# Kernel optimization log

Hardware: AMD Instinct MI355X
Metric: run time of the kernel (lower is better)

Reference implementation:

```python
import jax, jax.numpy as jnp
import numpy as np
import math

D_MODEL = 1024
NUM_HEADS = 16
D_KV = 64
INNER = NUM_HEADS * D_KV
NUM_BUCKETS = 32
MAX_DISTANCE = 128


def _relative_position_bucket(relative_position, num_buckets=NUM_BUCKETS, max_distance=MAX_DISTANCE):
    # bidirectional T5 bucketing
    n = -relative_position
    num_buckets = num_buckets // 2
    ret = (n < 0).astype(jnp.int32) * num_buckets
    n = jnp.abs(n)
    max_exact = num_buckets // 2
    is_small = n < max_exact
    n_safe = jnp.maximum(n, 1).astype(jnp.float32)  # avoid log(0); masked by is_small
    val_if_large = max_exact + (
        jnp.log(n_safe / max_exact) / math.log(max_distance / max_exact) * (num_buckets - max_exact)
    ).astype(jnp.int32)
    val_if_large = jnp.minimum(val_if_large, num_buckets - 1)
    return jnp.where(is_small, n, val_if_large) + ret


def _position_bias(rel_emb, q_len, k_len):
    ctx = jnp.arange(q_len)[:, None]
    mem = jnp.arange(k_len)[None, :]
    buckets = _relative_position_bucket(mem - ctx)          # [q, k]
    values = rel_emb[buckets]                               # [q, k, H]
    return jnp.transpose(values, (2, 0, 1))[None]           # [1, H, q, k]


def setup_inputs() -> dict:
    key = jax.random.key(0)
    ks = jax.random.split(key, 6)
    B, S = 2, 2048
    scale = 1.0 / math.sqrt(D_MODEL)
    return {
        "hidden_states": jax.random.normal(ks[0], (B, S, D_MODEL), dtype=jnp.float32),
        "mask": jnp.zeros((B, 1, 1, S), dtype=jnp.float32),
        "Wq": jax.random.normal(ks[1], (D_MODEL, INNER), dtype=jnp.float32) * scale,
        "Wk": jax.random.normal(ks[2], (D_MODEL, INNER), dtype=jnp.float32) * scale,
        "Wv": jax.random.normal(ks[3], (D_MODEL, INNER), dtype=jnp.float32) * scale,
        "Wo": jax.random.normal(ks[4], (INNER, D_MODEL), dtype=jnp.float32) * scale,
        "rel_emb": jax.random.normal(ks[5], (NUM_BUCKETS, NUM_HEADS), dtype=jnp.float32),
    }


def reference(hidden_states, mask, Wq, Wk, Wv, Wo, rel_emb):
    B, S, _ = hidden_states.shape
    def split_heads(x):
        return jnp.transpose(x.reshape(B, -1, NUM_HEADS, D_KV), (0, 2, 1, 3))  # [B,H,S,d]
    q = split_heads(hidden_states @ Wq)
    k = split_heads(hidden_states @ Wk)
    v = split_heads(hidden_states @ Wv)
    scores = jnp.einsum("bhqd,bhkd->bhqk", q, k)            # unscaled, T5-style
    position_bias = _position_bias(rel_emb, S, S)           # [1,H,S,S]
    scores = scores + position_bias + mask
    attn = jax.nn.softmax(scores, axis=-1)
    context = jnp.einsum("bhqk,bhkd->bhqd", attn, v)
    context = jnp.transpose(context, (0, 2, 1, 3)).reshape(B, S, INNER)
    output = context @ Wo
    return output, position_bias
```

## Files before the change

kernel.cpp:

```cpp
#include <hip/hip_runtime.h>
#include <cstdint>

#define AS1 __attribute__((address_space(1)))
#define AS3 __attribute__((address_space(3)))

typedef _Float16 half8 __attribute__((ext_vector_type(8)));
typedef _Float16 half4_t __attribute__((ext_vector_type(4)));
typedef float v4f __attribute__((ext_vector_type(4)));

__device__ __forceinline__ void async_ld16(const void* g, void* l) {
  __builtin_amdgcn_global_load_lds((const AS1 uint32_t*)g, (AS3 uint32_t*)l, 16, 0, 0);
}

__device__ __forceinline__ int t5_bucket(int delta) {
  int n = -delta;
  int ret = 0;
  if (n < 0) { ret = 16; n = -n; }
  if (n < 8) return n + ret;
  if (n >= 91) return 15 + ret;
  if ((n & (n - 1)) == 0) {
    int l = 31 - __clz(n);
    int v = 2 + 2 * l;
    return (v > 15 ? 15 : v) + ret;
  }
  int v = 8 + (int)(logf((float)n * 0.125f) * (8.0f / logf(16.0f)));
  return (v > 15 ? 15 : v) + ret;
}

__global__ void k_cvt(const float* __restrict__ src, _Float16* __restrict__ dst) {
  int t = blockIdx.x * 256 + threadIdx.x;
  float4 f = ((const float4*)src)[t];
  half4_t h = {(_Float16)f.x, (_Float16)f.y, (_Float16)f.z, (_Float16)f.w};
  ((half4_t*)dst)[t] = h;
}

__global__ void k_wt(const float* __restrict__ src, _Float16* __restrict__ dst) {
  __shared__ float tile[32][33];
  int tx = threadIdx.x, ty = threadIdx.y;
  int bx = blockIdx.x * 32, by = blockIdx.y * 32;
#pragma unroll
  for (int i = 0; i < 32; i += 8)
    tile[ty + i][tx] = src[(size_t)(by + ty + i) * 1024 + bx + tx];
  __syncthreads();
#pragma unroll
  for (int i = 0; i < 32; i += 8)
    dst[(size_t)(bx + ty + i) * 1024 + by + tx] = (_Float16)tile[tx][ty + i];
}

__global__ void k_vt(const _Float16* __restrict__ qkv, _Float16* __restrict__ vT) {
  __shared__ float tile[64 * 73];
  const int t = threadIdx.x;
  const int s0 = blockIdx.x * 64, h = blockIdx.y, b = blockIdx.z;
  const int r = t >> 2, c = (t & 3) * 16;
  const _Float16* src = qkv + (size_t)(b * 2048 + s0 + r) * 3072 + 2048 + h * 64 + c;
  half8 a0 = *(const half8*)src;
  half8 a1 = *(const half8*)(src + 8);
#pragma unroll
  for (int e = 0; e < 8; ++e) tile[r * 73 + c + e] = (float)a0[e];
#pragma unroll
  for (int e = 0; e < 8; ++e) tile[r * 73 + c + 8 + e] = (float)a1[e];
  __syncthreads();
  half8 w0, w1;
#pragma unroll
  for (int e = 0; e < 8; ++e) w0[e] = (_Float16)tile[(c + e) * 73 + r];
#pragma unroll
  for (int e = 0; e < 8; ++e) w1[e] = (_Float16)tile[(c + 8 + e) * 73 + r];
  _Float16* dst = vT + ((size_t)((b * 16 + h) * 64 + r)) * 2048 + s0 + c;
  *(half8*)dst = w0;
  *(half8*)(dst + 8) = w1;
}

__global__ void k_bias(const float* __restrict__ rel, float* __restrict__ outb) {
  __shared__ float tbl[512];
  int tid = threadIdx.x;
  tbl[tid] = rel[tid];
  tbl[tid + 256] = rel[tid + 256];
  __syncthreads();
  unsigned t = blockIdx.x * 256 + tid;
  int k4 = t & 511;
  int q = (t >> 9) & 2047;
  int h = t >> 20;
  int kb = k4 * 4;
  float4 v;
  if (kb - q >= 91) {
    float c = tbl[31 * 16 + h];
    v = make_float4(c, c, c, c);
  } else if (q - kb - 3 >= 91) {
    float c = tbl[15 * 16 + h];
    v = make_float4(c, c, c, c);
  } else {
    v.x = tbl[t5_bucket(kb + 0 - q) * 16 + h];
    v.y = tbl[t5_bucket(kb + 1 - q) * 16 + h];
    v.z = tbl[t5_bucket(kb + 2 - q) * 16 + h];
    v.w = tbl[t5_bucket(kb + 3 - q) * 16 + h];
  }
  ((float4*)outb)[((size_t)h * 2048 + q) * 512 + k4] = v;
}

template <bool F16OUT>
__global__ __launch_bounds__(256, 2) void k_gemm(const _Float16* __restrict__ A,
                                                 const _Float16* __restrict__ BT,
                                                 void* __restrict__ Cv, int K, int ldc) {
  __shared__ __align__(16) _Float16 As[128 * 32];
  __shared__ __align__(16) _Float16 Bs[128 * 32];
  const int tid = threadIdx.x;
  const int wave = tid >> 6, lane = tid & 63;
  const int l15 = lane & 15, quad = lane >> 4;
  const int m0 = blockIdx.y * 128, n0 = blockIdx.x * 128;
  const int wm = (wave >> 1) * 64, wn = (wave & 1) * 64;
  const int r0 = tid >> 2, c0 = (tid & 3) * 8;
  v4f acc[4][4] = {};
  for (int k0 = 0; k0 < K; k0 += 32) {
    __syncthreads();
    async_ld16(A + (size_t)(m0 + r0) * K + k0 + c0, (char*)As + (size_t)(wave * 64) * 16);
    async_ld16(A + (size_t)(m0 + 64 + r0) * K + k0 + c0,
               (char*)As + (size_t)(256 + wave * 64) * 16);
    async_ld16(BT + (size_t)(n0 + r0) * K + k0 + c0, (char*)Bs + (size_t)(wave * 64) * 16);
    async_ld16(BT + (size_t)(n0 + 64 + r0) * K + k0 + c0,
               (char*)Bs + (size_t)(256 + wave * 64) * 16);
    __syncthreads();
    half8 af[4], bf[4];
#pragma unroll
    for (int mt = 0; mt < 4; ++mt)
      af[mt] = *(const half8*)(As + (wm + mt * 16 + l15) * 32 + quad * 8);
#pragma unroll
    for (int nt = 0; nt < 4; ++nt)
      bf[nt] = *(const half8*)(Bs + (wn + nt * 16 + l15) * 32 + quad * 8);
#pragma unroll
    for (int mt = 0; mt < 4; ++mt)
#pragma unroll
      for (int nt = 0; nt < 4; ++nt)
        acc[mt][nt] = __builtin_amdgcn_mfma_f32_16x16x32_f16(af[mt], bf[nt], acc[mt][nt], 0, 0, 0);
  }
#pragma unroll
  for (int mt = 0; mt < 4; ++mt)
#pragma unroll
    for (int nt = 0; nt < 4; ++nt)
#pragma unroll
      for (int r = 0; r < 4; ++r) {
        int row = m0 + wm + mt * 16 + quad * 4 + r;
        int col = n0 + wn + nt * 16 + l15;
        if (F16OUT)
          ((_Float16*)Cv)[(size_t)row * ldc + col] = (_Float16)acc[mt][nt][r];
        else
          ((float*)Cv)[(size_t)row * ldc + col] = acc[mt][nt][r];
      }
}

__global__ __launch_bounds__(256, 2) void k_gemm_n64(const _Float16* __restrict__ A,
                                                     const _Float16* __restrict__ BT,
                                                     float* __restrict__ C, int K, int ldc) {
  __shared__ __align__(16) _Float16 As[128 * 32];
  __shared__ __align__(16) _Float16 Bs[64 * 32];
  const int tid = threadIdx.x;
  const int wave = tid >> 6, lane = tid & 63;
  const int l15 = lane & 15, quad = lane >> 4;
  const int m0 = blockIdx.y * 128, n0 = blockIdx.x * 64;
  const int wm = (wave >> 1) * 64, wn = (wave & 1) * 32;
  const int r0 = tid >> 2, c0 = (tid & 3) * 8;
  v4f acc[4][2] = {};
  for (int k0 = 0; k0 < K; k0 += 32) {
    __syncthreads();
    async_ld16(A + (size_t)(m0 + r0) * K + k0 + c0, (char*)As + (size_t)(wave * 64) * 16);
    async_ld16(A + (size_t)(m0 + 64 + r0) * K + k0 + c0,
               (char*)As + (size_t)(256 + wave * 64) * 16);
    async_ld16(BT + (size_t)(n0 + r0) * K + k0 + c0, (char*)Bs + (size_t)(wave * 64) * 16);
    __syncthreads();
    half8 af[4], bf[2];
#pragma unroll
    for (int mt = 0; mt < 4; ++mt)
      af[mt] = *(const half8*)(As + (wm + mt * 16 + l15) * 32 + quad * 8);
#pragma unroll
    for (int nt = 0; nt < 2; ++nt)
      bf[nt] = *(const half8*)(Bs + (wn + nt * 16 + l15) * 32 + quad * 8);
#pragma unroll
    for (int mt = 0; mt < 4; ++mt)
#pragma unroll
      for (int nt = 0; nt < 2; ++nt)
        acc[mt][nt] = __builtin_amdgcn_mfma_f32_16x16x32_f16(af[mt], bf[nt], acc[mt][nt], 0, 0, 0);
  }
#pragma unroll
  for (int mt = 0; mt < 4; ++mt)
#pragma unroll
    for (int nt = 0; nt < 2; ++nt)
#pragma unroll
      for (int r = 0; r < 4; ++r)
        C[(size_t)(m0 + wm + mt * 16 + quad * 4 + r) * ldc + n0 + wn + nt * 16 + l15] =
            acc[mt][nt][r];
}

__global__ __launch_bounds__(256, 3) void k_attn(const _Float16* __restrict__ qkv,
                                                 const _Float16* __restrict__ vT,
                                                 const float* __restrict__ mask,
                                                 const float* __restrict__ rel,
                                                 _Float16* __restrict__ ctx) {
  constexpr int S = 2048, LD = 3072;
  __shared__ __align__(16) _Float16 Ks[64 * 72];
  __shared__ __align__(16) _Float16 VT[64 * 72];
  __shared__ __align__(16) _Float16 Psh[128 * 72];
  __shared__ float btab[512];
  const int tid = threadIdx.x, wave = tid >> 6, lane = tid & 63;
  const int l15 = lane & 15, quad = lane >> 4;
  const int q0 = blockIdx.x * 128, h = blockIdx.y, b = blockIdx.z;

  for (int j = tid; j < 512; j += 256) btab[j] = rel[t5_bucket(j - 256) * 16 + h];
  const float c_past = rel[15 * 16 + h];
  const float c_fut = rel[31 * 16 + h];

  half8 bq[2][2];
#pragma unroll
  for (int qt = 0; qt < 2; ++qt) {
    const _Float16* qp = qkv + (size_t)(b * S + q0 + wave * 32 + qt * 16 + l15) * LD + h * 64;
    bq[qt][0] = *(const half8*)(qp + quad * 8);
    bq[qt][1] = *(const half8*)(qp + 32 + quad * 8);
  }
  v4f o[2][4] = {};
  float mrun[2] = {-INFINITY, -INFINITY};
  float lrun[2] = {0.f, 0.f};

  const int srow = tid >> 2, scol = (tid & 3) * 8;
  const _Float16* kg = qkv + (size_t)(b * S + srow) * LD + 1024 + h * 64 + scol;
  const _Float16* vg = vT + ((size_t)((b * 16 + h) * 64 + srow)) * S + scol;
  const float4* mkp = (const float4*)(mask + (size_t)b * S);

  for (int kv0 = 0; kv0 < S; kv0 += 64) {
    half8 kr0 = *(const half8*)(kg + (size_t)kv0 * LD);
    half8 kr1 = *(const half8*)(kg + (size_t)kv0 * LD + 32);
    half8 vr0 = *(const half8*)(vg + kv0);
    half8 vr1 = *(const half8*)(vg + kv0 + 32);
    float4 mk[4];
#pragma unroll
    for (int mt = 0; mt < 4; ++mt) mk[mt] = mkp[(kv0 >> 2) + mt * 4 + quad];
    __syncthreads();
    *(half8*)(Ks + srow * 72 + scol) = kr0;
    *(half8*)(Ks + srow * 72 + scol + 32) = kr1;
    *(half8*)(VT + srow * 72 + scol) = vr0;
    *(half8*)(VT + srow * 72 + scol + 32) = vr1;
    __syncthreads();

    v4f sc[2][4] = {};
#pragma unroll
    for (int kc = 0; kc < 2; ++kc)
#pragma unroll
      for (int mt = 0; mt < 4; ++mt) {
        half8 af = *(const half8*)(Ks + (mt * 16 + l15) * 72 + kc * 32 + quad * 8);
        sc[0][mt] = __builtin_amdgcn_mfma_f32_16x16x32_f16(af, bq[0][0 + kc], sc[0][mt], 0, 0, 0);
        sc[1][mt] = __builtin_amdgcn_mfma_f32_16x16x32_f16(af, bq[1][0 + kc], sc[1][mt], 0, 0, 0);
      }

    const int diff = kv0 - q0;
    const bool mixed = (diff >= -153) && (diff <= 217);
    const float cf = (diff >= 218) ? c_fut : c_past;
    v4f cm[4];
#pragma unroll
    for (int mt = 0; mt < 4; ++mt) {
      cm[mt][0] = mk[mt].x; cm[mt][1] = mk[mt].y; cm[mt][2] = mk[mt].z; cm[mt][3] = mk[mt].w;
      if (!mixed) {
        cm[mt][0] += cf; cm[mt][1] += cf; cm[mt][2] += cf; cm[mt][3] += cf;
      }
    }
    if (mixed) {
#pragma unroll
      for (int qt = 0; qt < 2; ++qt) {
        const int qq = q0 + wave * 32 + qt * 16 + l15;
#pragma unroll
        for (int mt = 0; mt < 4; ++mt) {
          int base = kv0 + mt * 16 + quad * 4 - qq + 256;
#pragma unroll
          for (int r = 0; r < 4; ++r) sc[qt][mt][r] += btab[base + r] + cm[mt][r];
        }
      }
    } else {
#pragma unroll
      for (int qt = 0; qt < 2; ++qt)
#pragma unroll
        for (int mt = 0; mt < 4; ++mt)
#pragma unroll
          for (int r = 0; r < 4; ++r) sc[qt][mt][r] += cm[mt][r];
    }

#pragma unroll
    for (int qt = 0; qt < 2; ++qt) {
      v4f m4 = sc[qt][0];
#pragma unroll
      for (int r = 0; r < 4; ++r) {
        m4[r] = fmaxf(m4[r], sc[qt][1][r]);
        m4[r] = fmaxf(m4[r], sc[qt][2][r]);
        m4[r] = fmaxf(m4[r], sc[qt][3][r]);
      }
      float mx = fmaxf(fmaxf(m4[0], m4[1]), fmaxf(m4[2], m4[3]));
      mx = fmaxf(mx, __shfl_xor(mx, 16, 64));
      mx = fmaxf(mx, __shfl_xor(mx, 32, 64));
      float mnew = fmaxf(mrun[qt], mx);
      float alpha = __expf(mrun[qt] - mnew);
      mrun[qt] = mnew;
      v4f s4 = {};
#pragma unroll
      for (int mt = 0; mt < 4; ++mt)
#pragma unroll
        for (int r = 0; r < 4; ++r) {
          float p = __expf(sc[qt][mt][r] - mnew);
          sc[qt][mt][r] = p;
          s4[r] += p;
        }
      float rs = (s4[0] + s4[1]) + (s4[2] + s4[3]);
      rs += __shfl_xor(rs, 16, 64);
      rs += __shfl_xor(rs, 32, 64);
      lrun[qt] = lrun[qt] * alpha + rs;
#pragma unroll
      for (int dt = 0; dt < 4; ++dt)
#pragma unroll
        for (int r = 0; r < 4; ++r) o[qt][dt][r] *= alpha;
      const int prow = wave * 32 + qt * 16 + l15;
#pragma unroll
      for (int mt = 0; mt < 4; ++mt) {
        half4_t ph = {(_Float16)sc[qt][mt][0], (_Float16)sc[qt][mt][1],
                      (_Float16)sc[qt][mt][2], (_Float16)sc[qt][mt][3]};
        *(half4_t*)(Psh + prow * 72 + mt * 16 + quad * 4) = ph;
      }
    }
    __syncthreads();

#pragma unroll
    for (int kc = 0; kc < 2; ++kc) {
      half8 bp0 = *(const half8*)(Psh + (wave * 32 + l15) * 72 + kc * 32 + quad * 8);
      half8 bp1 = *(const half8*)(Psh + (wave * 32 + 16 + l15) * 72 + kc * 32 + quad * 8);
#pragma unroll
      for (int dt = 0; dt < 4; ++dt) {
        half8 av = *(const half8*)(VT + (dt * 16 + l15) * 72 + kc * 32 + quad * 8);
        o[0][dt] = __builtin_amdgcn_mfma_f32_16x16x32_f16(av, bp0, o[0][dt], 0, 0, 0);
        o[1][dt] = __builtin_amdgcn_mfma_f32_16x16x32_f16(av, bp1, o[1][dt], 0, 0, 0);
      }
    }
  }
#pragma unroll
  for (int qt = 0; qt < 2; ++qt) {
    float inv = 1.0f / lrun[qt];
    const size_t token = (size_t)(b * S + q0 + wave * 32 + qt * 16 + l15);
#pragma unroll
    for (int dt = 0; dt < 4; ++dt) {
      half4_t hv = {(_Float16)(o[qt][dt][0] * inv), (_Float16)(o[qt][dt][1] * inv),
                    (_Float16)(o[qt][dt][2] * inv), (_Float16)(o[qt][dt][3] * inv)};
      *(half4_t*)(ctx + token * 1024 + h * 64 + dt * 16 + quad * 4) = hv;
    }
  }
}

extern "C" void kernel_launch(void* const* d_in, const int* in_sizes, int n_in,
                              void* d_out, int out_size, void* d_ws, size_t ws_size,
                              hipStream_t stream) {
  const float* hs = (const float*)d_in[0];
  const float* mask = (const float*)d_in[1];
  const float* Wq = (const float*)d_in[2];
  const float* Wk = (const float*)d_in[3];
  const float* Wv = (const float*)d_in[4];
  const float* Wo = (const float*)d_in[5];
  const float* rel = (const float*)d_in[6];
  float* out = (float*)d_out;

  char* ws = (char*)d_ws;
  _Float16* hsF = (_Float16*)(ws);
  _Float16* wqkvT = (_Float16*)(ws + (8u << 20));
  _Float16* woT = (_Float16*)(ws + (14u << 20));
  _Float16* qkv = (_Float16*)(ws + (16u << 20));
  _Float16* ctx = (_Float16*)(ws + (40u << 20));
  _Float16* vT = (_Float16*)(ws + (48u << 20));

  k_cvt<<<4096, 256, 0, stream>>>(hs, hsF);
  k_wt<<<dim3(32, 32), dim3(32, 8), 0, stream>>>(Wq, wqkvT);
  k_wt<<<dim3(32, 32), dim3(32, 8), 0, stream>>>(Wk, wqkvT + (1u << 20));
  k_wt<<<dim3(32, 32), dim3(32, 8), 0, stream>>>(Wv, wqkvT + (2u << 20));
  k_wt<<<dim3(32, 32), dim3(32, 8), 0, stream>>>(Wo, woT);

  k_gemm<true><<<dim3(24, 32), 256, 0, stream>>>(hsF, wqkvT, qkv, 1024, 3072);
  k_vt<<<dim3(32, 16, 2), 256, 0, stream>>>(qkv, vT);
  k_bias<<<65536, 256, 0, stream>>>(rel, out + 4194304);
  k_attn<<<dim3(16, 16, 2), 256, 0, stream>>>(qkv, vT, mask, rel, ctx);
  k_gemm_n64<<<dim3(16, 32), 256, 0, stream>>>(ctx, woT, out, 1024, 1024);
}
```

Baseline: 460.9 us.

## Fuse weight transposes, V-transpose into QKV GEMM, and bias writer into attention

Merges the four weight-transpose launches into one 3D-grid kernel. The QKV GEMM now writes the V columns straight into the transposed vT layout, which removes the separate k_vt pass. The position-bias writer is folded into the attention launch as extra blocks that fill the 64MB bias output while the attention blocks run, using the per-head btab lookup instead of recomputing t5_bucket per element. This cuts launch count and lets the bandwidth-heavy bias store overlap attention compute, at the cost of strided 8-byte vT stores and a non-uniform grid.

```diff
diff --git a/kernel.cpp b/kernel.cpp
--- a/kernel.cpp
+++ b/kernel.cpp
@@ -34,8 +34,13 @@
   ((half4_t*)dst)[t] = h;
 }
 
-__global__ void k_wt(const float* __restrict__ src, _Float16* __restrict__ dst) {
+__global__ void k_wt_all(const float* __restrict__ Wq, const float* __restrict__ Wk,
+                         const float* __restrict__ Wv, const float* __restrict__ Wo,
+                         _Float16* __restrict__ wqkvT, _Float16* __restrict__ woT) {
   __shared__ float tile[32][33];
+  const int z = blockIdx.z;
+  const float* src = (z == 0) ? Wq : (z == 1) ? Wk : (z == 2) ? Wv : Wo;
+  _Float16* dst = (z < 3) ? (wqkvT + ((size_t)z << 20)) : woT;
   int tx = threadIdx.x, ty = threadIdx.y;
   int bx = blockIdx.x * 32, by = blockIdx.y * 32;
 #pragma unroll
@@ -47,60 +52,11 @@
     dst[(size_t)(bx + ty + i) * 1024 + by + tx] = (_Float16)tile[tx][ty + i];
 }
 
-__global__ void k_vt(const _Float16* __restrict__ qkv, _Float16* __restrict__ vT) {
-  __shared__ float tile[64 * 73];
-  const int t = threadIdx.x;
-  const int s0 = blockIdx.x * 64, h = blockIdx.y, b = blockIdx.z;
-  const int r = t >> 2, c = (t & 3) * 16;
-  const _Float16* src = qkv + (size_t)(b * 2048 + s0 + r) * 3072 + 2048 + h * 64 + c;
-  half8 a0 = *(const half8*)src;
-  half8 a1 = *(const half8*)(src + 8);
-#pragma unroll
-  for (int e = 0; e < 8; ++e) tile[r * 73 + c + e] = (float)a0[e];
-#pragma unroll
-  for (int e = 0; e < 8; ++e) tile[r * 73 + c + 8 + e] = (float)a1[e];
-  __syncthreads();
-  half8 w0, w1;
-#pragma unroll
-  for (int e = 0; e < 8; ++e) w0[e] = (_Float16)tile[(c + e) * 73 + r];
-#pragma unroll
-  for (int e = 0; e < 8; ++e) w1[e] = (_Float16)tile[(c + 8 + e) * 73 + r];
-  _Float16* dst = vT + ((size_t)((b * 16 + h) * 64 + r)) * 2048 + s0 + c;
-  *(half8*)dst = w0;
-  *(half8*)(dst + 8) = w1;
-}
-
-__global__ void k_bias(const float* __restrict__ rel, float* __restrict__ outb) {
-  __shared__ float tbl[512];
-  int tid = threadIdx.x;
-  tbl[tid] = rel[tid];
-  tbl[tid + 256] = rel[tid + 256];
-  __syncthreads();
-  unsigned t = blockIdx.x * 256 + tid;
-  int k4 = t & 511;
-  int q = (t >> 9) & 2047;
-  int h = t >> 20;
-  int kb = k4 * 4;
-  float4 v;
-  if (kb - q >= 91) {
-    float c = tbl[31 * 16 + h];
-    v = make_float4(c, c, c, c);
-  } else if (q - kb - 3 >= 91) {
-    float c = tbl[15 * 16 + h];
-    v = make_float4(c, c, c, c);
-  } else {
-    v.x = tbl[t5_bucket(kb + 0 - q) * 16 + h];
-    v.y = tbl[t5_bucket(kb + 1 - q) * 16 + h];
-    v.z = tbl[t5_bucket(kb + 2 - q) * 16 + h];
-    v.w = tbl[t5_bucket(kb + 3 - q) * 16 + h];
-  }
-  ((float4*)outb)[((size_t)h * 2048 + q) * 512 + k4] = v;
-}
-
 template <bool F16OUT>
 __global__ __launch_bounds__(256, 2) void k_gemm(const _Float16* __restrict__ A,
                                                  const _Float16* __restrict__ BT,
-                                                 void* __restrict__ Cv, int K, int ldc) {
+                                                 void* __restrict__ Cv,
+                                                 _Float16* __restrict__ vT, int K, int ldc) {
   __shared__ __align__(16) _Float16 As[128 * 32];
   __shared__ __align__(16) _Float16 Bs[128 * 32];
   const int tid = threadIdx.x;
@@ -131,6 +87,20 @@
 #pragma unroll
       for (int nt = 0; nt < 4; ++nt)
         acc[mt][nt] = __builtin_amdgcn_mfma_f32_16x16x32_f16(af[mt], bf[nt], acc[mt][nt], 0, 0, 0);
+  }
+  if (F16OUT && n0 >= 2048) {
+#pragma unroll
+    for (int mt = 0; mt < 4; ++mt)
+#pragma unroll
+      for (int nt = 0; nt < 4; ++nt) {
+        int col = n0 + wn + nt * 16 + l15 - 2048;
+        int row0 = m0 + wm + mt * 16 + quad * 4;
+        int bb = row0 >> 11, s0 = row0 & 2047;
+        half4_t hv = {(_Float16)acc[mt][nt][0], (_Float16)acc[mt][nt][1],
+                      (_Float16)acc[mt][nt][2], (_Float16)acc[mt][nt][3]};
+        *(half4_t*)(vT + ((size_t)bb * 1024 + col) * 2048 + s0) = hv;
+      }
+    return;
   }
 #pragma unroll
   for (int mt = 0; mt < 4; ++mt)
@@ -189,11 +159,12 @@
             acc[mt][nt][r];
 }
 
-__global__ __launch_bounds__(256, 3) void k_attn(const _Float16* __restrict__ qkv,
-                                                 const _Float16* __restrict__ vT,
-                                                 const float* __restrict__ mask,
-                                                 const float* __restrict__ rel,
-                                                 _Float16* __restrict__ ctx) {
+__global__ __launch_bounds__(256, 3) void k_attn_bias(const _Float16* __restrict__ qkv,
+                                                      const _Float16* __restrict__ vT,
+                                                      const float* __restrict__ mask,
+                                                      const float* __restrict__ rel,
+                                                      _Float16* __restrict__ ctx,
+                                                      float* __restrict__ outb) {
   constexpr int S = 2048, LD = 3072;
   __shared__ __align__(16) _Float16 Ks[64 * 72];
   __shared__ __align__(16) _Float16 VT[64 * 72];
@@ -201,11 +172,39 @@
   __shared__ float btab[512];
   const int tid = threadIdx.x, wave = tid >> 6, lane = tid & 63;
   const int l15 = lane & 15, quad = lane >> 4;
-  const int q0 = blockIdx.x * 128, h = blockIdx.y, b = blockIdx.z;
+  const int h = blockIdx.y, b = blockIdx.z;
 
   for (int j = tid; j < 512; j += 256) btab[j] = rel[t5_bucket(j - 256) * 16 + h];
   const float c_past = rel[15 * 16 + h];
   const float c_fut = rel[31 * 16 + h];
+  __syncthreads();
+
+  if (blockIdx.x >= 16) {
+    const int blk = blockIdx.x - 16;
+    float4* op = (float4*)outb + (size_t)h * 2048 * 512;
+#pragma unroll 4
+    for (int i = 0; i < 256; ++i) {
+      int idx = blk * 65536 + i * 256 + tid;
+      int k4 = idx & 511;
+      int q = b * 1024 + (idx >> 9);
+      int kb = k4 * 4;
+      float4 v;
+      if (kb - q >= 91) {
+        v = make_float4(c_fut, c_fut, c_fut, c_fut);
+      } else if (q - kb - 3 >= 91) {
+        v = make_float4(c_past, c_past, c_past, c_past);
+      } else {
+        v.x = btab[kb + 0 - q + 256];
+        v.y = btab[kb + 1 - q + 256];
+        v.z = btab[kb + 2 - q + 256];
+        v.w = btab[kb + 3 - q + 256];
+      }
+      op[(size_t)q * 512 + k4] = v;
+    }
+    return;
+  }
+
+  const int q0 = blockIdx.x * 128;
 
   half8 bq[2][2];
 #pragma unroll
@@ -244,8 +243,8 @@
 #pragma unroll
       for (int mt = 0; mt < 4; ++mt) {
         half8 af = *(const half8*)(Ks + (mt * 16 + l15) * 72 + kc * 32 + quad * 8);
-        sc[0][mt] = __builtin_amdgcn_mfma_f32_16x16x32_f16(af, bq[0][0 + kc], sc[0][mt], 0, 0, 0);
-        sc[1][mt] = __builtin_amdgcn_mfma_f32_16x16x32_f16(af, bq[1][0 + kc], sc[1][mt], 0, 0, 0);
+        sc[0][mt] = __builtin_amdgcn_mfma_f32_16x16x32_f16(af, bq[0][kc], sc[0][mt], 0, 0, 0);
+        sc[1][mt] = __builtin_amdgcn_mfma_f32_16x16x32_f16(af, bq[1][kc], sc[1][mt], 0, 0, 0);
       }
 
     const int diff = kv0 - q0;
@@ -367,14 +366,9 @@
   _Float16* vT = (_Float16*)(ws + (48u << 20));
 
   k_cvt<<<4096, 256, 0, stream>>>(hs, hsF);
-  k_wt<<<dim3(32, 32), dim3(32, 8), 0, stream>>>(Wq, wqkvT);
-  k_wt<<<dim3(32, 32), dim3(32, 8), 0, stream>>>(Wk, wqkvT + (1u << 20));
-  k_wt<<<dim3(32, 32), dim3(32, 8), 0, stream>>>(Wv, wqkvT + (2u << 20));
-  k_wt<<<dim3(32, 32), dim3(32, 8), 0, stream>>>(Wo, woT);
-
-  k_gemm<true><<<dim3(24, 32), 256, 0, stream>>>(hsF, wqkvT, qkv, 1024, 3072);
-  k_vt<<<dim3(32, 16, 2), 256, 0, stream>>>(qkv, vT);
-  k_bias<<<65536, 256, 0, stream>>>(rel, out + 4194304);
-  k_attn<<<dim3(16, 16, 2), 256, 0, stream>>>(qkv, vT, mask, rel, ctx);
+  k_wt_all<<<dim3(32, 32, 4), dim3(32, 8), 0, stream>>>(Wq, Wk, Wv, Wo, wqkvT, woT);
+
+  k_gemm<true><<<dim3(24, 32), 256, 0, stream>>>(hsF, wqkvT, qkv, vT, 1024, 3072);
+  k_attn_bias<<<dim3(24, 16, 2), 256, 0, stream>>>(qkv, vT, mask, rel, ctx, out + 4194304);
   k_gemm_n64<<<dim3(16, 32), 256, 0, stream>>>(ctx, woT, out, 1024, 1024);
 }
```

Measured after the change: 436.9 us. 5.2% less time.
